# Kernel optimization log

Measured on AMD Instinct MI355X. Metric: run time of the kernel, lower is better.

The kernel has to match this reference:

```python
import jax, jax.numpy as jnp
import numpy as np
import math

B, S, D, H, F = 4, 1024, 1024, 16, 4096
NUM_BUCKETS, MAX_DISTANCE = 32, 128
LN_EPS = 1e-5


def _relative_position_bucket(relative_position, num_buckets=NUM_BUCKETS, max_distance=MAX_DISTANCE):
    # bidirectional T5 bucketing, faithful to the torch source
    n = -relative_position
    num_buckets = num_buckets // 2  # 16
    ret = (n < 0).astype(jnp.int32) * num_buckets
    n = jnp.abs(n)
    max_exact = num_buckets // 2  # 8
    is_small = n < max_exact
    val_if_large = max_exact + (
        jnp.log(jnp.maximum(n, 1).astype(jnp.float32) / max_exact)
        / math.log(max_distance / max_exact)
        * (num_buckets - max_exact)
    ).astype(jnp.int32)
    val_if_large = jnp.minimum(val_if_large, num_buckets - 1)
    return ret + jnp.where(is_small, n, val_if_large)


def layer_norm(x, g, b):
    mu = jnp.mean(x, axis=-1, keepdims=True)
    var = jnp.mean((x - mu) ** 2, axis=-1, keepdims=True)
    return g * (x - mu) / jnp.sqrt(var + LN_EPS) + b


def setup_inputs() -> dict:
    key = jax.random.key(0)
    ks = jax.random.split(key, 12)
    s = 0.02
    return {
        "in_state": jax.random.normal(ks[0], (B, S, D), jnp.float32),
        "padding_mask": jnp.ones((B, S), jnp.int32),
        "Wq": jax.random.normal(ks[1], (D, D), jnp.float32) * s,
        "bq": jnp.zeros((D,), jnp.float32),
        "Wk": jax.random.normal(ks[2], (D, D), jnp.float32) * s,
        "bk": jnp.zeros((D,), jnp.float32),
        "Wv": jax.random.normal(ks[3], (D, D), jnp.float32) * s,
        "bv": jnp.zeros((D,), jnp.float32),
        "Wo": jax.random.normal(ks[4], (D, D), jnp.float32) * s,
        "bo": jnp.zeros((D,), jnp.float32),
        "rel_bias": jax.random.normal(ks[5], (NUM_BUCKETS, H), jnp.float32) * s,
        "ln1_g": jnp.ones((D,), jnp.float32),
        "ln1_b": jnp.zeros((D,), jnp.float32),
        "W1": jax.random.normal(ks[6], (D, F), jnp.float32) * s,
        "b1": jnp.zeros((F,), jnp.float32),
        "W2": jax.random.normal(ks[7], (F, D), jnp.float32) * s,
        "b2": jnp.zeros((D,), jnp.float32),
        "ln2_g": jnp.ones((D,), jnp.float32),
        "ln2_b": jnp.zeros((D,), jnp.float32),
    }


def reference(in_state, padding_mask, Wq, bq, Wk, bk, Wv, bv, Wo, bo, rel_bias,
              ln1_g, ln1_b, W1, b1, W2, b2, ln2_g, ln2_b):
    b, s, d = in_state.shape
    dh = d // H
    q = in_state @ Wq + bq
    k = in_state @ Wk + bk
    v = in_state @ Wv + bv
    # faithful to torch's q.view(B*H, S, d_head) flat reshape (no head transpose)
    qh = q.reshape(b * H, s, dh)
    kh = k.reshape(b * H, s, dh)
    vh = v.reshape(b * H, s, dh)
    scores = jnp.einsum('bqd,bkd->bqk', qh, kh)  # no 1/sqrt(d) scaling (T5 style)
    # relative position bias: [H, S, S] tiled over batch -> block index b*H+h gets head h
    rel_pos = jnp.arange(s)[:, None] - jnp.arange(s)[None, :]
    buckets = _relative_position_bucket(rel_pos)
    bias = rel_bias[buckets].transpose(2, 0, 1)  # [H, S, S]
    bias = jnp.tile(bias, (b, 1, 1))  # [B*H, S, S]
    # padding mask: log(0/1) -> -inf/0; block b*H+h uses mask[b, value_index]
    pad = jnp.log(padding_mask.astype(jnp.float32))  # [B, S]
    pad = jnp.repeat(pad, H, axis=0)[:, None, :]  # [B*H, 1, S]
    attw = jax.nn.softmax(scores + bias + pad, axis=-1)
    att = (attw @ vh).reshape(b, s, d)
    att = att @ Wo + bo
    h = layer_norm(att + in_state, ln1_g, ln1_b)
    ff = jnp.maximum(h @ W1 + b1, 0.0) @ W2 + b2
    out = layer_norm(ff + h, ln2_g, ln2_b)
    return out
```

## Files before the change

kernel.cpp:

```cpp
#include <hip/hip_runtime.h>
#include <hip/hip_bf16.h>

typedef unsigned short u16;
typedef __attribute__((ext_vector_type(8))) short bhalf8;
typedef __attribute__((ext_vector_type(4))) float f32x4;

#define DEV __device__ __forceinline__

DEV float bf2f(u16 u) { union { unsigned int i; float f; } c; c.i = ((unsigned int)u) << 16; return c.f; }
DEV u16 f2bf(float f) {
  union { float f; unsigned int i; } c; c.f = f;
  unsigned int x = c.i;
  x += 0x7fffu + ((x >> 16) & 1u);
  return (u16)(x >> 16);
}

DEV void async16(const void* g, void* l) {
  __builtin_amdgcn_global_load_lds((__attribute__((address_space(1))) void*)g,
                                   (__attribute__((address_space(3))) void*)l, 16, 0, 0);
}

DEV void atom_pk_bf16(void* p, unsigned int v) {
  asm volatile("global_atomic_pk_add_bf16 %0, %1, off" :: "v"(p), "v"(v) : "memory");
}

struct Ptr11 { const void* p[11]; };
struct TC4 { const void* in[4]; u16* out[4]; };

__global__ void detect_kernel(const unsigned int* __restrict__ x, int* __restrict__ flag) {
  int t = threadIdx.x;
  int cnt = 0;
  for (int i = t; i < 256; i += 64) {
    unsigned int w = x[i];
    int e = (w >> 7) & 0xFF;
    if (e >= 96 && e <= 134) cnt++;
  }
#pragma unroll
  for (int o = 1; o < 64; o <<= 1) cnt += __shfl_xor(cnt, o, 64);
  if (t == 0) *flag = (cnt >= 192) ? 1 : 0;
}

DEV bhalf8 load8B(const void* base, size_t e, int isbf) {
  if (isbf) return *(const bhalf8*)((const u16*)base + e);
  const float* f = (const float*)base + e;
  float4 a = *(const float4*)f;
  float4 b = *(const float4*)(f + 4);
  bhalf8 r;
  r[0] = (short)f2bf(a.x); r[1] = (short)f2bf(a.y); r[2] = (short)f2bf(a.z); r[3] = (short)f2bf(a.w);
  r[4] = (short)f2bf(b.x); r[5] = (short)f2bf(b.y); r[6] = (short)f2bf(b.z); r[7] = (short)f2bf(b.w);
  return r;
}

__global__ __launch_bounds__(256) void convert_x(const void* __restrict__ x,
                                                 u16* __restrict__ dst,
                                                 const int* __restrict__ flag) {
  int c = blockIdx.x * 256 + threadIdx.x;
  u16* d = dst + (size_t)c * 4;
  if (*flag) {
    *(ushort4*)d = ((const ushort4*)x)[c];
  } else {
    float4 v = ((const float4*)x)[c];
    d[0] = f2bf(v.x); d[1] = f2bf(v.y); d[2] = f2bf(v.z); d[3] = f2bf(v.w);
  }
}

__global__ __launch_bounds__(256) void convert_small(Ptr11 s, float* __restrict__ dst,
                                                     const int* __restrict__ flag) {
  const int isbf = *flag;
  const int SZ[11] = {1024,1024,1024,1024,512,1024,1024,4096,1024,1024,1024};
  for (int i = threadIdx.x; i < 13824; i += 256) {
    int acc = 0, seg = -1, off = 0;
#pragma unroll
    for (int s2 = 0; s2 < 11; ++s2) {
      if (seg < 0 && i < acc + SZ[s2]) { seg = s2; off = i - acc; }
      acc += SZ[s2];
    }
    dst[i] = isbf ? bf2f(((const u16*)s.p[seg])[off]) : ((const float*)s.p[seg])[off];
  }
}

__global__ __launch_bounds__(256) void bias_init(const float* __restrict__ bias,
                                                 u16* __restrict__ out) {
  const int row = blockIdx.x, t = threadIdx.x;
  float4 bv = *(const float4*)(bias + t * 4);
  ushort4 ov; ov.x = f2bf(bv.x); ov.y = f2bf(bv.y); ov.z = f2bf(bv.z); ov.w = f2bf(bv.w);
  *(ushort4*)(out + (size_t)row * 1024 + t * 4) = ov;
}

DEV void tconv_tile(const void* in, u16* out, int R, int C, int isbf) {
  __shared__ __align__(16) u16 tile[64][72];
  const int t = threadIdx.x;
  const int c0 = blockIdx.x * 64, r0 = blockIdx.y * 64;
#pragma unroll
  for (int r = 0; r < 2; ++r) {
    int idx = r * 256 + t;
    int ri = idx >> 3, cc = (idx & 7) * 8;
    bhalf8 v = load8B(in, (size_t)(r0 + ri) * C + c0 + cc, isbf);
    *(bhalf8*)(&tile[ri][cc]) = v;
  }
  __syncthreads();
#pragma unroll
  for (int r = 0; r < 2; ++r) {
    int idx = r * 256 + t;
    int co = idx >> 3, rc = (idx & 7) * 8;
    bhalf8 v;
#pragma unroll
    for (int ii = 0; ii < 8; ++ii) v[ii] = (short)tile[rc + ii][co];
    *(bhalf8*)(out + (size_t)(c0 + co) * R + r0 + rc) = v;
  }
}

__global__ __launch_bounds__(256) void tconv_w4(TC4 p, const int* __restrict__ flag) {
  int z = blockIdx.z;
  tconv_tile(p.in[z], p.out[z], 1024, 1024, *flag);
}

__global__ __launch_bounds__(256) void tconv_generic(const void* in, u16* out, int R, int C,
                                                     const int* __restrict__ flag) {
  tconv_tile(in, out, R, C, *flag);
}

__global__ __launch_bounds__(256) void transpose_generic(const u16* in, u16* out, int R, int C) {
  __shared__ __align__(16) u16 tile[64][72];
  const int t = threadIdx.x;
  const int c0 = blockIdx.x * 64, r0 = blockIdx.y * 64;
  size_t bs = (size_t)R * C * blockIdx.z;
#pragma unroll
  for (int r = 0; r < 2; ++r) {
    int idx = r * 256 + t;
    int ri = idx >> 3, cc = (idx & 7) * 8;
    *(bhalf8*)(&tile[ri][cc]) = *(const bhalf8*)(in + bs + (size_t)(r0 + ri) * C + c0 + cc);
  }
  __syncthreads();
#pragma unroll
  for (int r = 0; r < 2; ++r) {
    int idx = r * 256 + t;
    int co = idx >> 3, rc = (idx & 7) * 8;
    bhalf8 v;
#pragma unroll
    for (int ii = 0; ii < 8; ++ii) v[ii] = (short)tile[rc + ii][co];
    *(bhalf8*)(out + bs + (size_t)(c0 + co) * R + r0 + rc) = v;
  }
}

#define MFMA_BF16(a, b, c) __builtin_amdgcn_mfma_f32_16x16x32_bf16(a, b, c, 0, 0, 0)

template<int RELU, int ATOMIC>
__global__ __launch_bounds__(512) void gemm256(
    const u16* __restrict__ A, const u16* __restrict__ BT0,
    const float* __restrict__ b0, const float* __restrict__ b1, const float* __restrict__ b2,
    u16* __restrict__ C0, int M, int N, int ldk, int kext, long sBT, long sC)
{
  __shared__ __align__(16) u16 ldsAll[65536];
  (void)M;

  const int t = threadIdx.x;
  const int wv = t >> 6, l = t & 63;
  const int wm = wv >> 2, wn = wv & 3;
  const int m0 = blockIdx.y * 256, n0 = blockIdx.x * 256;
  const int z = blockIdx.z;

  const u16* BT; const float* bias; u16* C; int koff;
  if (ATOMIC) {
    BT = BT0; bias = b0; C = C0; koff = z * kext;
  } else {
    BT = BT0 + (long)z * sBT;
    bias = (z == 0) ? b0 : (z == 1 ? b1 : b2);
    C = C0 + (long)z * sC;
    koff = 0;
  }

  const int ri = t >> 3;
  const int slc8 = (((t & 7) ^ (ri & 7)) << 3);
  const u16* agp = A + (size_t)(m0 + ri) * ldk + koff + slc8;
  const int rB = ((ri >> 5) << 6) | (ri & 31);
  const u16* bgp = BT + (size_t)(n0 + rB) * ldk + koff + slc8;

  char* lbase = (char*)ldsAll;
  char* ldst = lbase + wv * 1024;

#define STG_A(bufb, h, j, kt) async16(agp + (size_t)((j) * 128 + (h) * 64) * ldk + (size_t)(kt) * 64, \
                                      ldst + (bufb) * 32768 + (h) * 16384 + (j) * 8192)
#define STG_B(bufb, h, j, kt) async16(bgp + (size_t)((j) * 128 + (h) * 32) * ldk + (size_t)(kt) * 64, \
                                      ldst + 65536 + (bufb) * 32768 + (h) * 16384 + (j) * 8192)

  int offA[4][2], offB[2][2];
#pragma unroll
  for (int mi = 0; mi < 4; ++mi)
#pragma unroll
    for (int s = 0; s < 2; ++s)
      offA[mi][s] = wm * 8192 + (mi * 16 + (l & 15)) * 128 + ((((s << 2) + (l >> 4)) ^ (l & 7)) << 4);
#pragma unroll
  for (int nj = 0; nj < 2; ++nj)
#pragma unroll
    for (int s = 0; s < 2; ++s)
      offB[nj][s] = 65536 + wn * 4096 + (nj * 16 + (l & 15)) * 128 + ((((s << 2) + (l >> 4)) ^ (l & 7)) << 4);

  const int NT = kext >> 6;
  f32x4 acc[8][4] = {};

  STG_A(0, 0, 0, 0); STG_A(0, 0, 1, 0);
  STG_B(0, 0, 0, 0); STG_B(0, 0, 1, 0);
  STG_B(0, 1, 0, 0); STG_B(0, 1, 1, 0);
  STG_A(0, 1, 0, 0); STG_A(0, 1, 1, 0);
  if (NT > 1) {
    STG_A(1, 0, 0, 1); STG_A(1, 0, 1, 1);
    STG_B(1, 0, 0, 1); STG_B(1, 0, 1, 1);
    STG_B(1, 1, 0, 1); STG_B(1, 1, 1, 1);
    asm volatile("s_waitcnt vmcnt(6)" ::: "memory");
  } else {
    asm volatile("s_waitcnt vmcnt(0)" ::: "memory");
  }
  __builtin_amdgcn_s_barrier();

  for (int tt = 0; tt < NT; ++tt) {
    const int bf = tt & 1;
    const int bo = bf << 15;
    bhalf8 af[4][2], p0[2][2], p1[2][2];

#pragma unroll
    for (int mi = 0; mi < 4; ++mi)
#pragma unroll
      for (int s = 0; s < 2; ++s)
        af[mi][s] = *(const bhalf8*)(lbase + bo + offA[mi][s]);
#pragma unroll
    for (int nj = 0; nj < 2; ++nj)
#pragma unroll
      for (int s = 0; s < 2; ++s)
        p0[nj][s] = *(const bhalf8*)(lbase + bo + offB[nj][s]);
    if (tt + 1 < NT) { STG_A(bf ^ 1, 1, 0, tt + 1); STG_A(bf ^ 1, 1, 1, tt + 1); }
    __builtin_amdgcn_s_barrier();
    asm volatile("s_waitcnt lgkmcnt(0)" ::: "memory");
    __builtin_amdgcn_s_setprio(1);
#pragma unroll
    for (int mi = 0; mi < 4; ++mi)
#pragma unroll
      for (int nj = 0; nj < 2; ++nj) {
        acc[mi][nj] = MFMA_BF16(af[mi][0], p0[nj][0], acc[mi][nj]);
        acc[mi][nj] = MFMA_BF16(af[mi][1], p0[nj][1], acc[mi][nj]);
      }
    __builtin_amdgcn_s_setprio(0);
    __builtin_amdgcn_s_barrier();

#pragma unroll
    for (int nj = 0; nj < 2; ++nj)
#pragma unroll
      for (int s = 0; s < 2; ++s)
        p1[nj][s] = *(const bhalf8*)(lbase + bo + 16384 + offB[nj][s]);
    if (tt + 2 < NT) { STG_A(bf, 0, 0, tt + 2); STG_A(bf, 0, 1, tt + 2); }
    __builtin_amdgcn_s_barrier();
    asm volatile("s_waitcnt lgkmcnt(0)" ::: "memory");
    __builtin_amdgcn_s_setprio(1);
#pragma unroll
    for (int mi = 0; mi < 4; ++mi)
#pragma unroll
      for (int nj = 0; nj < 2; ++nj) {
        acc[mi][2 + nj] = MFMA_BF16(af[mi][0], p1[nj][0], acc[mi][2 + nj]);
        acc[mi][2 + nj] = MFMA_BF16(af[mi][1], p1[nj][1], acc[mi][2 + nj]);
      }
    __builtin_amdgcn_s_setprio(0);
    __builtin_amdgcn_s_barrier();

#pragma unroll
    for (int mi = 0; mi < 4; ++mi)
#pragma unroll
      for (int s = 0; s < 2; ++s)
        af[mi][s] = *(const bhalf8*)(lbase + bo + 16384 + offA[mi][s]);
    if (tt + 2 < NT) { STG_B(bf, 0, 0, tt + 2); STG_B(bf, 0, 1, tt + 2); }
    __builtin_amdgcn_s_barrier();
    asm volatile("s_waitcnt lgkmcnt(0)" ::: "memory");
    __builtin_amdgcn_s_setprio(1);
#pragma unroll
    for (int mi = 0; mi < 4; ++mi)
#pragma unroll
      for (int nj = 0; nj < 2; ++nj) {
        acc[4 + mi][2 + nj] = MFMA_BF16(af[mi][0], p1[nj][0], acc[4 + mi][2 + nj]);
        acc[4 + mi][2 + nj] = MFMA_BF16(af[mi][1], p1[nj][1], acc[4 + mi][2 + nj]);
      }
    __builtin_amdgcn_s_setprio(0);
    __builtin_amdgcn_s_barrier();

    if (tt + 2 < NT) { STG_B(bf, 1, 0, tt + 2); STG_B(bf, 1, 1, tt + 2); }
    __builtin_amdgcn_s_barrier();
    __builtin_amdgcn_s_setprio(1);
#pragma unroll
    for (int mi = 0; mi < 4; ++mi)
#pragma unroll
      for (int nj = 0; nj < 2; ++nj) {
        acc[4 + mi][nj] = MFMA_BF16(af[mi][0], p0[nj][0], acc[4 + mi][nj]);
        acc[4 + mi][nj] = MFMA_BF16(af[mi][1], p0[nj][1], acc[4 + mi][nj]);
      }
    __builtin_amdgcn_s_setprio(0);
    if (tt < NT - 2) {
      asm volatile("s_waitcnt vmcnt(6)" ::: "memory");
    } else if (tt == NT - 2) {
      asm volatile("s_waitcnt vmcnt(0)" ::: "memory");
    }
    __builtin_amdgcn_s_barrier();
  }
#undef STG_A
#undef STG_B

  const int lr = (l >> 4) << 2, lcc = l & 15;
  if (ATOMIC) {
#pragma unroll
    for (int nj = 0; nj < 4; ++nj) {
      int col = n0 + wn * 64 + nj * 16 + lcc;
#pragma unroll
      for (int mi = 0; mi < 8; ++mi) {
#pragma unroll
        for (int r = 0; r < 4; ++r) {
          int row = m0 + wm * 128 + mi * 16 + lr + r;
          float vo = acc[mi][nj][r];
          float vn = __shfl_xor(vo, 1, 64);
          if (!(l & 1)) {
            unsigned int pk = (unsigned int)f2bf(vo) | ((unsigned int)f2bf(vn) << 16);
            atom_pk_bf16((void*)(C + (size_t)row * N + col), pk);
          }
        }
      }
    }
  } else {
#pragma unroll
    for (int nj = 0; nj < 4; ++nj) {
      int col = n0 + wn * 64 + nj * 16 + lcc;
      float bb = bias[col];
#pragma unroll
      for (int mi = 0; mi < 8; ++mi) {
#pragma unroll
        for (int r = 0; r < 4; ++r) {
          int row = m0 + wm * 128 + mi * 16 + lr + r;
          float v = acc[mi][nj][r] + bb;
          if (RELU) v = fmaxf(v, 0.0f);
          C[(size_t)row * N + col] = f2bf(v);
        }
      }
    }
  }
}

template<int RELU>
__global__ __launch_bounds__(512) void gemm_bt(
    const u16* __restrict__ A, const u16* __restrict__ BT0,
    const float* __restrict__ b0, const float* __restrict__ b1, const float* __restrict__ b2,
    u16* __restrict__ C0, int M, int N, int K, long sBT, long sC)
{
  __shared__ __align__(16) u16 ldsA[128 * 32];
  __shared__ __align__(16) u16 ldsB[128 * 32];

  const int t = threadIdx.x;
  const int wv = t >> 6, l = t & 63;
  const int wm = wv >> 2, wn = wv & 3;
  const int m0 = blockIdx.y * 128, n0 = blockIdx.x * 128;
  const int z = blockIdx.z;

  const u16* BT = BT0 + (long)z * sBT;
  const float* bias = (z == 0) ? b0 : (z == 1 ? b1 : b2);
  u16* C = C0 + (long)z * sC;

  const int mm_s = t >> 2, kc_s = (t & 3) ^ ((t >> 4) & 3);
  const u16* agp = A + (size_t)(m0 + mm_s) * K + kc_s * 8;
  const u16* bgp = BT + (size_t)(n0 + mm_s) * K + kc_s * 8;
  char* la = (char*)ldsA + wv * 1024;
  char* lb = (char*)ldsB + wv * 1024;

  int a_off[4], b_off[2];
#pragma unroll
  for (int i = 0; i < 4; ++i) {
    int mm = wm * 64 + i * 16 + (l & 15);
    a_off[i] = (mm * 4 + ((l >> 4) ^ ((mm >> 2) & 3))) * 8;
  }
#pragma unroll
  for (int j = 0; j < 2; ++j) {
    int nn = wn * 32 + j * 16 + (l & 15);
    b_off[j] = (nn * 4 + ((l >> 4) ^ ((nn >> 2) & 3))) * 8;
  }

  f32x4 acc[4][2] = {};

  for (int kt = 0; kt < K; kt += 32) {
    __syncthreads();
    async16(agp + kt, la);
    async16(bgp + kt, lb);
    __syncthreads();

    bhalf8 af[4], bfr[2];
#pragma unroll
    for (int i = 0; i < 4; ++i) af[i] = *(const bhalf8*)(ldsA + a_off[i]);
#pragma unroll
    for (int j = 0; j < 2; ++j) bfr[j] = *(const bhalf8*)(ldsB + b_off[j]);
#pragma unroll
    for (int mi = 0; mi < 4; ++mi)
#pragma unroll
      for (int nj = 0; nj < 2; ++nj)
        acc[mi][nj] = __builtin_amdgcn_mfma_f32_16x16x32_bf16(af[mi], bfr[nj], acc[mi][nj], 0, 0, 0);
  }

  const int lr = (l >> 4) << 2, lc = l & 15;
#pragma unroll
  for (int nj = 0; nj < 2; ++nj) {
    int col = n0 + wn * 32 + nj * 16 + lc;
    float bb = bias[col];
#pragma unroll
    for (int mi = 0; mi < 4; ++mi) {
#pragma unroll
      for (int r = 0; r < 4; ++r) {
        int row = m0 + wm * 64 + mi * 16 + lr + r;
        float v = acc[mi][nj][r] + bb;
        if (RELU) v = fmaxf(v, 0.0f);
        C[(size_t)row * N + col] = f2bf(v);
      }
    }
  }
}

template<int RELU>
__global__ __launch_bounds__(256) void gemm_bn(
    const u16* __restrict__ A, const void* __restrict__ B,
    const float* __restrict__ bias, u16* __restrict__ C, int M, int N, int K,
    const int* __restrict__ flag)
{
  __shared__ __align__(16) u16 ldsA[128][40];
  __shared__ __align__(16) u16 ldsB[128][40];

  const int isbf = *flag;
  const int t = threadIdx.x;
  const int wv = t >> 6, l = t & 63;
  const int wm = wv & 1, wn = wv >> 1;
  const int m0 = blockIdx.y * 128, n0 = blockIdx.x * 128;

  const int srow = t >> 1, scol = (t & 1) * 16;
  const u16* agp = A + (size_t)(m0 + srow) * K + scol;

  const int kk = t >> 3;
  const int nn = (t & 7) * 16;

  f32x4 acc[4][4] = {};

  for (int kt = 0; kt < K; kt += 32) {
    bhalf8 a0 = *(const bhalf8*)(agp + kt);
    bhalf8 a1 = *(const bhalf8*)(agp + kt + 8);
    size_t e0 = (size_t)(kt + kk) * N + n0 + nn;
    bhalf8 b0v = load8B(B, e0, isbf);
    bhalf8 b1v = load8B(B, e0 + 8, isbf);
    __syncthreads();
    *(bhalf8*)(&ldsA[srow][scol])     = a0;
    *(bhalf8*)(&ldsA[srow][scol + 8]) = a1;
#pragma unroll
    for (int j = 0; j < 8; ++j) ldsB[nn + j][kk]     = (u16)b0v[j];
#pragma unroll
    for (int j = 0; j < 8; ++j) ldsB[nn + 8 + j][kk] = (u16)b1v[j];
    __syncthreads();

    bhalf8 af[4], bfr[4];
#pragma unroll
    for (int i = 0; i < 4; ++i)
      af[i] = *(const bhalf8*)(&ldsA[wm * 64 + i * 16 + (l & 15)][(l >> 4) * 8]);
#pragma unroll
    for (int i = 0; i < 4; ++i)
      bfr[i] = *(const bhalf8*)(&ldsB[wn * 64 + i * 16 + (l & 15)][(l >> 4) * 8]);
#pragma unroll
    for (int mi = 0; mi < 4; ++mi)
#pragma unroll
      for (int ni = 0; ni < 4; ++ni)
        acc[mi][ni] = __builtin_amdgcn_mfma_f32_16x16x32_bf16(af[mi], bfr[ni], acc[mi][ni], 0, 0, 0);
  }

  const int lr = (l >> 4) << 2, lc = l & 15;
#pragma unroll
  for (int ni = 0; ni < 4; ++ni) {
    int col = n0 + wn * 64 + ni * 16 + lc;
    float bb = bias[col];
#pragma unroll
    for (int mi = 0; mi < 4; ++mi) {
#pragma unroll
      for (int r = 0; r < 4; ++r) {
        int row = m0 + wm * 64 + mi * 16 + lr + r;
        float v = acc[mi][ni][r] + bb;
        if (RELU) v = fmaxf(v, 0.0f);
        C[(size_t)row * N + col] = f2bf(v);
      }
    }
  }
}

__global__ __launch_bounds__(256) void lut_kernel(const float* __restrict__ rbc, float* __restrict__ lut) {
  int idx = blockIdx.x * 256 + threadIdx.x;
  if (idx >= 16 * 2047) return;
  int h = idx / 2047;
  int dp = idx - h * 2047;
  int delta = dp - 1023;
  int n = -delta;
  int ret = 0;
  if (n < 0) { ret = 16; n = -n; }
  int bkt;
  if (n < 8) bkt = n;
  else {
    float v = logf((float)n * 0.125f) / logf(16.0f) * 8.0f;
    bkt = 8 + (int)v;
    if (bkt > 15) bkt = 15;
  }
  lut[idx] = (rbc[(ret + bkt) * 16 + h] - 12.0f) * 1.44269504f;
}

__global__ __launch_bounds__(256) void attn_fused(
    const u16* __restrict__ q, const u16* __restrict__ k, const u16* __restrict__ vt,
    const int* __restrict__ mask, const float* __restrict__ lut, u16* __restrict__ att)
{
  __shared__ __align__(16) u16 ldsQ[64][72];
  __shared__ __align__(16) u16 ldsK[64][72];
  __shared__ __align__(16) u16 ldsV[64][72];
  __shared__ __align__(16) u16 ldsP[4][16][72];
  __shared__ float ldsLut[2047];
  __shared__ float ldsPad[64];

  const int t = threadIdx.x;
  const int wv = t >> 6, l = t & 63;
  const int bh = blockIdx.x, qt = blockIdx.y;
  const int b = bh >> 4, h = bh & 15;
  const size_t base = (size_t)bh * 65536;
  const int q0 = qt * 64;

  for (int i = t; i < 2047; i += 256) ldsLut[i] = lut[h * 2047 + i];

  const int sr = t >> 2, sc = (t & 3) * 16;
  {
    bhalf8 q0v = *(const bhalf8*)(q + base + (size_t)(q0 + sr) * 64 + sc);
    bhalf8 q1v = *(const bhalf8*)(q + base + (size_t)(q0 + sr) * 64 + sc + 8);
    *(bhalf8*)(&ldsQ[sr][sc])     = q0v;
    *(bhalf8*)(&ldsQ[sr][sc + 8]) = q1v;
  }
  __syncthreads();

  bhalf8 qf[2];
  {
    int mm = wv * 16 + (l & 15);
#pragma unroll
    for (int s = 0; s < 2; ++s)
      qf[s] = *(const bhalf8*)(&ldsQ[mm][s * 32 + (l >> 4) * 8]);
  }

  float ls_part[4] = {0.0f, 0.0f, 0.0f, 0.0f};
  f32x4 acc_o[4] = {};

  const int* mrow = mask + b * 1024;

  for (int kt = 0; kt < 16; ++kt) {
    const int k0 = kt * 64;
    bhalf8 k0v = *(const bhalf8*)(k + base + (size_t)(k0 + sr) * 64 + sc);
    bhalf8 k1v = *(const bhalf8*)(k + base + (size_t)(k0 + sr) * 64 + sc + 8);
    bhalf8 v0v = *(const bhalf8*)(vt + base + (size_t)sr * 1024 + k0 + sc);
    bhalf8 v1v = *(const bhalf8*)(vt + base + (size_t)sr * 1024 + k0 + sc + 8);
    __syncthreads();
    *(bhalf8*)(&ldsK[sr][sc])     = k0v;
    *(bhalf8*)(&ldsK[sr][sc + 8]) = k1v;
    *(bhalf8*)(&ldsV[sr][sc])     = v0v;
    *(bhalf8*)(&ldsV[sr][sc + 8]) = v1v;
    if (t < 64) {
      int mv = mrow[k0 + t];
      ldsPad[t] = (mv > 0) ? __log2f((float)mv) : -1e30f;
    }
    __syncthreads();

    f32x4 accS[4] = {};
#pragma unroll
    for (int s = 0; s < 2; ++s) {
#pragma unroll
      for (int ni = 0; ni < 4; ++ni) {
        int nnj = ni * 16 + (l & 15);
        bhalf8 kf = *(const bhalf8*)(&ldsK[nnj][s * 32 + (l >> 4) * 8]);
        accS[ni] = __builtin_amdgcn_mfma_f32_16x16x32_bf16(qf[s], kf, accS[ni], 0, 0, 0);
      }
    }

    float padv[4];
#pragma unroll
    for (int ni = 0; ni < 4; ++ni) padv[ni] = ldsPad[ni * 16 + (l & 15)];
    const int ib = q0 + wv * 16 + ((l >> 4) << 2);
#pragma unroll
    for (int r = 0; r < 4; ++r) {
      int i_l = ((l >> 4) << 2) + r;
#pragma unroll
      for (int ni = 0; ni < 4; ++ni) {
        int j_l = ni * 16 + (l & 15);
        float s = fmaf(accS[ni][r], 1.44269504f, ldsLut[(ib + r) - (k0 + j_l) + 1023]) + padv[ni];
        float p = exp2f(s);
        ls_part[r] += p;
        ldsP[wv][i_l][j_l] = f2bf(p);
      }
    }

#pragma unroll
    for (int s = 0; s < 2; ++s) {
      int mm = l & 15;
      bhalf8 pf = *(const bhalf8*)(&ldsP[wv][mm][s * 32 + (l >> 4) * 8]);
#pragma unroll
      for (int ni = 0; ni < 4; ++ni) {
        int e = ni * 16 + (l & 15);
        bhalf8 vf = *(const bhalf8*)(&ldsV[e][s * 32 + (l >> 4) * 8]);
        acc_o[ni] = __builtin_amdgcn_mfma_f32_16x16x32_bf16(pf, vf, acc_o[ni], 0, 0, 0);
      }
    }
  }

#pragma unroll
  for (int r = 0; r < 4; ++r) {
#pragma unroll
    for (int off = 1; off < 16; off <<= 1) ls_part[r] += __shfl_xor(ls_part[r], off, 64);
    ls_part[r] = 1.0f / ls_part[r];
  }

#pragma unroll
  for (int ni = 0; ni < 4; ++ni) {
#pragma unroll
    for (int r = 0; r < 4; ++r) {
      int i = q0 + wv * 16 + ((l >> 4) << 2) + r;
      int e = ni * 16 + (l & 15);
      att[base + (size_t)i * 64 + e] = f2bf(acc_o[ni][r] * ls_part[r]);
    }
  }
}

template<int LAST>
__global__ __launch_bounds__(256) void ln_kernel(
    const u16* __restrict__ x, const u16* __restrict__ res,
    const float* __restrict__ g, const float* __restrict__ b,
    void* __restrict__ out, const int* __restrict__ flag)
{
  const int row = blockIdx.x, t = threadIdx.x;
  const size_t off = (size_t)row * 1024 + t * 4;
  ushort4 xv = *(const ushort4*)(x + off);
  ushort4 rv = *(const ushort4*)(res + off);
  float v0 = bf2f(xv.x) + bf2f(rv.x);
  float v1 = bf2f(xv.y) + bf2f(rv.y);
  float v2 = bf2f(xv.z) + bf2f(rv.z);
  float v3 = bf2f(xv.w) + bf2f(rv.w);
  float s = v0 + v1 + v2 + v3;
  float sq = v0 * v0 + v1 * v1 + v2 * v2 + v3 * v3;
#pragma unroll
  for (int o = 1; o < 64; o <<= 1) { s += __shfl_xor(s, o, 64); sq += __shfl_xor(sq, o, 64); }
  __shared__ float red[8];
  const int wv = t >> 6, l = t & 63;
  if (l == 0) { red[wv] = s; red[4 + wv] = sq; }
  __syncthreads();
  s = red[0] + red[1] + red[2] + red[3];
  sq = red[4] + red[5] + red[6] + red[7];
  float mu = s * 0.0009765625f;
  float var = sq * 0.0009765625f - mu * mu;
  float rstd = rsqrtf(var + 1e-5f);
  float4 gv = *(const float4*)(g + t * 4);
  float4 bv = *(const float4*)(b + t * 4);
  float o0 = gv.x * (v0 - mu) * rstd + bv.x;
  float o1 = gv.y * (v1 - mu) * rstd + bv.y;
  float o2 = gv.z * (v2 - mu) * rstd + bv.z;
  float o3 = gv.w * (v3 - mu) * rstd + bv.w;
  if (!LAST) {
    ushort4 ov; ov.x = f2bf(o0); ov.y = f2bf(o1); ov.z = f2bf(o2); ov.w = f2bf(o3);
    *(ushort4*)((u16*)out + off) = ov;
  } else {
    if (*flag) {
      ushort4 ov; ov.x = f2bf(o0); ov.y = f2bf(o1); ov.z = f2bf(o2); ov.w = f2bf(o3);
      *(ushort4*)((u16*)out + off) = ov;
    } else {
      float4 ov; ov.x = o0; ov.y = o1; ov.z = o2; ov.w = o3;
      *(float4*)((float*)out + off) = ov;
    }
  }
}

extern "C" void kernel_launch(void* const* d_in, const int* in_sizes, int n_in,
                              void* d_out, int out_size, void* d_ws, size_t ws_size,
                              hipStream_t stream) {
  const void* x  = d_in[0];
  const int* mask = (const int*)d_in[1];
  const void* Wq = d_in[2];  const void* bq = d_in[3];
  const void* Wk = d_in[4];  const void* bk = d_in[5];
  const void* Wv = d_in[6];  const void* bv = d_in[7];
  const void* Wo = d_in[8];  const void* bo = d_in[9];
  const void* rb = d_in[10];
  const void* g1 = d_in[11]; const void* be1 = d_in[12];
  const void* W1 = d_in[13]; const void* b1 = d_in[14];
  const void* W2 = d_in[15]; const void* b2 = d_in[16];
  const void* g2 = d_in[17]; const void* be2 = d_in[18];

  char* ws = (char*)d_ws;
  const size_t MB = 1024 * 1024;
  const bool FAST = (ws_size >= 57 * MB);

  const size_t TAIL = FAST ? 56 * MB : 48 * MB;
  float* smalls = (float*)(ws + TAIL);
  float* lut    = (float*)(ws + TAIL + 56 * 1024);
  int*   flag   = (int*)(ws + TAIL + 192 * 1024);

  float* bqc  = smalls + 0;
  float* bkc  = smalls + 1024;
  float* bvc  = smalls + 2048;
  float* boc  = smalls + 3072;
  float* rbc  = smalls + 4096;
  float* g1c  = smalls + 4608;
  float* be1c = smalls + 5632;
  float* b1c  = smalls + 6656;
  float* b2c  = smalls + 10752;
  float* g2c  = smalls + 11776;
  float* be2c = smalls + 12800;

  detect_kernel<<<1, 64, 0, stream>>>((const unsigned int*)x, flag);
  Ptr11 sml;
  sml.p[0] = bq; sml.p[1] = bk; sml.p[2] = bv; sml.p[3] = bo; sml.p[4] = rb;
  sml.p[5] = g1; sml.p[6] = be1; sml.p[7] = b1; sml.p[8] = b2; sml.p[9] = g2; sml.p[10] = be2;
  convert_small<<<1, 256, 0, stream>>>(sml, smalls, flag);
  lut_kernel<<<dim3(128), 256, 0, stream>>>(rbc, lut);

  if (FAST) {
    u16* xc   = (u16*)(ws + 0 * MB);
    u16* WqT  = (u16*)(ws + 8 * MB);
    u16* WkT  = WqT + 1048576;
    u16* WvT  = WqT + 2 * 1048576;
    u16* WoT  = WqT + 3 * 1048576;
    u16* qb   = (u16*)(ws + 16 * MB);
    u16* kb   = (u16*)(ws + 24 * MB);
    u16* vb   = (u16*)(ws + 32 * MB);
    u16* vtb  = (u16*)(ws + 40 * MB);
    u16* attb = (u16*)(ws + 32 * MB);
    u16* xo   = (u16*)(ws + 16 * MB);
    u16* hb   = (u16*)(ws + 48 * MB);
    u16* W1T  = (u16*)(ws + 8 * MB);
    u16* W2T  = (u16*)(ws + 0 * MB);
    u16* ff1  = (u16*)(ws + 16 * MB);
    u16* ff2o = (u16*)(ws + 8 * MB);

    convert_x<<<4096, 256, 0, stream>>>(x, xc, flag);
    TC4 tw; tw.in[0] = Wq; tw.in[1] = Wk; tw.in[2] = Wv; tw.in[3] = Wo;
    tw.out[0] = WqT; tw.out[1] = WkT; tw.out[2] = WvT; tw.out[3] = WoT;
    tconv_w4<<<dim3(16, 16, 4), 256, 0, stream>>>(tw, flag);

    gemm_bt<0><<<dim3(8, 32, 3), 512, 0, stream>>>(xc, WqT, bqc, bkc, bvc, qb,
                                                   4096, 1024, 1024, 1048576L, 4194304L);
    transpose_generic<<<dim3(1, 16, 64), 256, 0, stream>>>(vb, vtb, 1024, 64);
    attn_fused<<<dim3(64, 16), 256, 0, stream>>>(qb, kb, vtb, mask, lut, attb);
    gemm_bt<0><<<dim3(8, 32, 1), 512, 0, stream>>>(attb, WoT, boc, boc, boc, xo,
                                                   4096, 1024, 1024, 0L, 0L);
    tconv_generic<<<dim3(64, 16), 256, 0, stream>>>(W1, W1T, 1024, 4096, flag);
    ln_kernel<0><<<dim3(4096), 256, 0, stream>>>(xo, xc, g1c, be1c, hb, flag);
    tconv_generic<<<dim3(16, 64), 256, 0, stream>>>(W2, W2T, 4096, 1024, flag);
    gemm256<1, 0><<<dim3(16, 16, 1), 512, 0, stream>>>(hb, W1T, b1c, b1c, b1c, ff1,
                                                       4096, 4096, 1024, 1024, 0L, 0L);
    bias_init<<<dim3(4096), 256, 0, stream>>>(b2c, ff2o);
    gemm256<0, 1><<<dim3(4, 16, 4), 512, 0, stream>>>(ff1, W2T, b2c, b2c, b2c, ff2o,
                                                      4096, 1024, 4096, 1024, 0L, 0L);
    ln_kernel<1><<<dim3(4096), 256, 0, stream>>>(ff2o, hb, g2c, be2c, d_out, flag);
  } else {
    u16* xc   = (u16*)(ws + 0 * MB);
    u16* WqT  = (u16*)(ws + 8 * MB);
    u16* WkT  = WqT + 1048576;
    u16* WvT  = WqT + 2 * 1048576;
    u16* WoT  = WqT + 3 * 1048576;
    u16* qb   = (u16*)(ws + 16 * MB);
    u16* kb   = (u16*)(ws + 24 * MB);
    u16* vb   = (u16*)(ws + 32 * MB);
    u16* vtb  = (u16*)(ws + 40 * MB);
    u16* attb = (u16*)(ws + 32 * MB);
    u16* xo   = (u16*)(ws + 16 * MB);
    u16* hb   = (u16*)(ws + 40 * MB);
    u16* ff1  = (u16*)(ws + 0 * MB);
    u16* ff2o = (u16*)(ws + 32 * MB);

    convert_x<<<4096, 256, 0, stream>>>(x, xc, flag);
    TC4 tw; tw.in[0] = Wq; tw.in[1] = Wk; tw.in[2] = Wv; tw.in[3] = Wo;
    tw.out[0] = WqT; tw.out[1] = WkT; tw.out[2] = WvT; tw.out[3] = WoT;
    tconv_w4<<<dim3(16, 16, 4), 256, 0, stream>>>(tw, flag);

    gemm_bt<0><<<dim3(8, 32, 3), 512, 0, stream>>>(xc, WqT, bqc, bkc, bvc, qb,
                                                   4096, 1024, 1024, 1048576L, 4194304L);
    transpose_generic<<<dim3(1, 16, 64), 256, 0, stream>>>(vb, vtb, 1024, 64);
    attn_fused<<<dim3(64, 16), 256, 0, stream>>>(qb, kb, vtb, mask, lut, attb);
    gemm_bt<0><<<dim3(8, 32, 1), 512, 0, stream>>>(attb, WoT, boc, boc, boc, xo,
                                                   4096, 1024, 1024, 0L, 0L);
    ln_kernel<0><<<dim3(4096), 256, 0, stream>>>(xo, xc, g1c, be1c, hb, flag);
    gemm_bn<1><<<dim3(32, 32), 256, 0, stream>>>(hb, W1, b1c, ff1, 4096, 4096, 1024, flag);
    gemm_bn<0><<<dim3(8, 32), 256, 0, stream>>>(ff1, W2, b2c, ff2o, 4096, 1024, 4096, flag);
    ln_kernel<1><<<dim3(4096), 256, 0, stream>>>(ff2o, hb, g2c, be2c, d_out, flag);
  }
}
```

Baseline: 445.1 us.

## Use separate LDS arrays in gemm256 and route QKV/out-proj GEMMs through it

```diff
diff --git a/kernel.cpp b/kernel.cpp
--- a/kernel.cpp
+++ b/kernel.cpp
@@ -151,7 +151,8 @@
     const float* __restrict__ b0, const float* __restrict__ b1, const float* __restrict__ b2,
     u16* __restrict__ C0, int M, int N, int ldk, int kext, long sBT, long sC)
 {
-  __shared__ __align__(16) u16 ldsAll[65536];
+  __shared__ __align__(16) u16 A0h0[8192], A0h1[8192], A1h0[8192], A1h1[8192];
+  __shared__ __align__(16) u16 B0h0[8192], B0h1[8192], B1h0[8192], B1h1[8192];
   (void)M;
 
   const int t = threadIdx.x;
@@ -176,13 +177,10 @@
   const int rB = ((ri >> 5) << 6) | (ri & 31);
   const u16* bgp = BT + (size_t)(n0 + rB) * ldk + koff + slc8;
 
-  char* lbase = (char*)ldsAll;
-  char* ldst = lbase + wv * 1024;
-
-#define STG_A(bufb, h, j, kt) async16(agp + (size_t)((j) * 128 + (h) * 64) * ldk + (size_t)(kt) * 64, \
-                                      ldst + (bufb) * 32768 + (h) * 16384 + (j) * 8192)
-#define STG_B(bufb, h, j, kt) async16(bgp + (size_t)((j) * 128 + (h) * 32) * ldk + (size_t)(kt) * 64, \
-                                      ldst + 65536 + (bufb) * 32768 + (h) * 16384 + (j) * 8192)
+#define STGA(ARR, h, j, kt) async16(agp + (size_t)((j) * 128 + (h) * 64) * ldk + (size_t)(kt) * 64, \
+                                    (char*)(ARR) + (j) * 8192 + wv * 1024)
+#define STGB(ARR, h, j, kt) async16(bgp + (size_t)((j) * 128 + (h) * 32) * ldk + (size_t)(kt) * 64, \
+                                    (char*)(ARR) + (j) * 8192 + wv * 1024)
 
   int offA[4][2], offB[2][2];
 #pragma unroll
@@ -194,112 +192,98 @@
   for (int nj = 0; nj < 2; ++nj)
 #pragma unroll
     for (int s = 0; s < 2; ++s)
-      offB[nj][s] = 65536 + wn * 4096 + (nj * 16 + (l & 15)) * 128 + ((((s << 2) + (l >> 4)) ^ (l & 7)) << 4);
+      offB[nj][s] = wn * 4096 + (nj * 16 + (l & 15)) * 128 + ((((s << 2) + (l >> 4)) ^ (l & 7)) << 4);
 
   const int NT = kext >> 6;
   f32x4 acc[8][4] = {};
 
-  STG_A(0, 0, 0, 0); STG_A(0, 0, 1, 0);
-  STG_B(0, 0, 0, 0); STG_B(0, 0, 1, 0);
-  STG_B(0, 1, 0, 0); STG_B(0, 1, 1, 0);
-  STG_A(0, 1, 0, 0); STG_A(0, 1, 1, 0);
+  STGA(A0h0, 0, 0, 0); STGA(A0h0, 0, 1, 0);
+  STGB(B0h0, 0, 0, 0); STGB(B0h0, 0, 1, 0);
+  STGB(B0h1, 1, 0, 0); STGB(B0h1, 1, 1, 0);
+  STGA(A0h1, 1, 0, 0); STGA(A0h1, 1, 1, 0);
   if (NT > 1) {
-    STG_A(1, 0, 0, 1); STG_A(1, 0, 1, 1);
-    STG_B(1, 0, 0, 1); STG_B(1, 0, 1, 1);
-    STG_B(1, 1, 0, 1); STG_B(1, 1, 1, 1);
+    STGA(A1h0, 0, 0, 1); STGA(A1h0, 0, 1, 1);
+    STGB(B1h0, 0, 0, 1); STGB(B1h0, 0, 1, 1);
+    STGB(B1h1, 1, 0, 1); STGB(B1h1, 1, 1, 1);
     asm volatile("s_waitcnt vmcnt(6)" ::: "memory");
   } else {
     asm volatile("s_waitcnt vmcnt(0)" ::: "memory");
   }
   __builtin_amdgcn_s_barrier();
 
-  for (int tt = 0; tt < NT; ++tt) {
-    const int bf = tt & 1;
-    const int bo = bf << 15;
-    bhalf8 af[4][2], p0[2][2], p1[2][2];
-
-#pragma unroll
-    for (int mi = 0; mi < 4; ++mi)
-#pragma unroll
-      for (int s = 0; s < 2; ++s)
-        af[mi][s] = *(const bhalf8*)(lbase + bo + offA[mi][s]);
-#pragma unroll
-    for (int nj = 0; nj < 2; ++nj)
-#pragma unroll
-      for (int s = 0; s < 2; ++s)
-        p0[nj][s] = *(const bhalf8*)(lbase + bo + offB[nj][s]);
-    if (tt + 1 < NT) { STG_A(bf ^ 1, 1, 0, tt + 1); STG_A(bf ^ 1, 1, 1, tt + 1); }
-    __builtin_amdgcn_s_barrier();
-    asm volatile("s_waitcnt lgkmcnt(0)" ::: "memory");
-    __builtin_amdgcn_s_setprio(1);
-#pragma unroll
-    for (int mi = 0; mi < 4; ++mi)
-#pragma unroll
-      for (int nj = 0; nj < 2; ++nj) {
-        acc[mi][nj] = MFMA_BF16(af[mi][0], p0[nj][0], acc[mi][nj]);
-        acc[mi][nj] = MFMA_BF16(af[mi][1], p0[nj][1], acc[mi][nj]);
-      }
-    __builtin_amdgcn_s_setprio(0);
-    __builtin_amdgcn_s_barrier();
-
-#pragma unroll
-    for (int nj = 0; nj < 2; ++nj)
-#pragma unroll
-      for (int s = 0; s < 2; ++s)
-        p1[nj][s] = *(const bhalf8*)(lbase + bo + 16384 + offB[nj][s]);
-    if (tt + 2 < NT) { STG_A(bf, 0, 0, tt + 2); STG_A(bf, 0, 1, tt + 2); }
-    __builtin_amdgcn_s_barrier();
-    asm volatile("s_waitcnt lgkmcnt(0)" ::: "memory");
-    __builtin_amdgcn_s_setprio(1);
-#pragma unroll
-    for (int mi = 0; mi < 4; ++mi)
-#pragma unroll
-      for (int nj = 0; nj < 2; ++nj) {
-        acc[mi][2 + nj] = MFMA_BF16(af[mi][0], p1[nj][0], acc[mi][2 + nj]);
-        acc[mi][2 + nj] = MFMA_BF16(af[mi][1], p1[nj][1], acc[mi][2 + nj]);
-      }
-    __builtin_amdgcn_s_setprio(0);
-    __builtin_amdgcn_s_barrier();
-
-#pragma unroll
-    for (int mi = 0; mi < 4; ++mi)
-#pragma unroll
-      for (int s = 0; s < 2; ++s)
-        af[mi][s] = *(const bhalf8*)(lbase + bo + 16384 + offA[mi][s]);
-    if (tt + 2 < NT) { STG_B(bf, 0, 0, tt + 2); STG_B(bf, 0, 1, tt + 2); }
-    __builtin_amdgcn_s_barrier();
-    asm volatile("s_waitcnt lgkmcnt(0)" ::: "memory");
-    __builtin_amdgcn_s_setprio(1);
-#pragma unroll
-    for (int mi = 0; mi < 4; ++mi)
-#pragma unroll
-      for (int nj = 0; nj < 2; ++nj) {
-        acc[4 + mi][2 + nj] = MFMA_BF16(af[mi][0], p1[nj][0], acc[4 + mi][2 + nj]);
-        acc[4 + mi][2 + nj] = MFMA_BF16(af[mi][1], p1[nj][1], acc[4 + mi][2 + nj]);
-      }
-    __builtin_amdgcn_s_setprio(0);
-    __builtin_amdgcn_s_barrier();
-
-    if (tt + 2 < NT) { STG_B(bf, 1, 0, tt + 2); STG_B(bf, 1, 1, tt + 2); }
-    __builtin_amdgcn_s_barrier();
-    __builtin_amdgcn_s_setprio(1);
-#pragma unroll
-    for (int mi = 0; mi < 4; ++mi)
-#pragma unroll
-      for (int nj = 0; nj < 2; ++nj) {
-        acc[4 + mi][nj] = MFMA_BF16(af[mi][0], p0[nj][0], acc[4 + mi][nj]);
-        acc[4 + mi][nj] = MFMA_BF16(af[mi][1], p0[nj][1], acc[4 + mi][nj]);
-      }
-    __builtin_amdgcn_s_setprio(0);
-    if (tt < NT - 2) {
-      asm volatile("s_waitcnt vmcnt(6)" ::: "memory");
-    } else if (tt == NT - 2) {
-      asm volatile("s_waitcnt vmcnt(0)" ::: "memory");
-    }
-    __builtin_amdgcn_s_barrier();
-  }
-#undef STG_A
-#undef STG_B
+#define ITER(TT, CA0, CA1, CB0, CB1, NA1)                                        \
+  {                                                                              \
+    bhalf8 af[4][2], p0[2][2], p1[2][2];                                         \
+                      \
+    _Pragma("unroll") for (int mi = 0; mi < 4; ++mi)                             \
+      _Pragma("unroll") for (int s = 0; s < 2; ++s)                              \
+        af[mi][s] = *(const bhalf8*)((const char*)(CA0) + offA[mi][s]);          \
+    _Pragma("unroll") for (int nj = 0; nj < 2; ++nj)                             \
+      _Pragma("unroll") for (int s = 0; s < 2; ++s)                              \
+        p0[nj][s] = *(const bhalf8*)((const char*)(CB0) + offB[nj][s]);          \
+    if ((TT) + 1 < NT) { STGA(NA1, 1, 0, (TT) + 1); STGA(NA1, 1, 1, (TT) + 1); } \
+    __builtin_amdgcn_s_barrier();                                                \
+    asm volatile("s_waitcnt lgkmcnt(0)" ::: "memory");                           \
+    __builtin_amdgcn_s_setprio(1);                                               \
+    _Pragma("unroll") for (int mi = 0; mi < 4; ++mi)                             \
+      _Pragma("unroll") for (int nj = 0; nj < 2; ++nj) {                         \
+        acc[mi][nj] = MFMA_BF16(af[mi][0], p0[nj][0], acc[mi][nj]);              \
+        acc[mi][nj] = MFMA_BF16(af[mi][1], p0[nj][1], acc[mi][nj]);              \
+      }                                                                          \
+    __builtin_amdgcn_s_setprio(0);                                               \
+    __builtin_amdgcn_s_barrier();                                                \
+                           \
+    _Pragma("unroll") for (int nj = 0; nj < 2; ++nj)                             \
+      _Pragma("unroll") for (int s = 0; s < 2; ++s)                              \
+        p1[nj][s] = *(const bhalf8*)((const char*)(CB1) + offB[nj][s]);          \
+    if ((TT) + 2 < NT) { STGA(CA0, 0, 0, (TT) + 2); STGA(CA0, 0, 1, (TT) + 2); } \
+    __builtin_amdgcn_s_barrier();                                                \
+    asm volatile("s_waitcnt lgkmcnt(0)" ::: "memory");                           \
+    __builtin_amdgcn_s_setprio(1);                                               \
+    _Pragma("unroll") for (int mi = 0; mi < 4; ++mi)                             \
+      _Pragma("unroll") for (int nj = 0; nj < 2; ++nj) {                         \
+        acc[mi][2 + nj] = MFMA_BF16(af[mi][0], p1[nj][0], acc[mi][2 + nj]);      \
+        acc[mi][2 + nj] = MFMA_BF16(af[mi][1], p1[nj][1], acc[mi][2 + nj]);      \
+      }                                                                          \
+    __builtin_amdgcn_s_setprio(0);                                               \
+    __builtin_amdgcn_s_barrier();                                                \
+                           \
+    _Pragma("unroll") for (int mi = 0; mi < 4; ++mi)                             \
+      _Pragma("unroll") for (int s = 0; s < 2; ++s)                              \
+        af[mi][s] = *(const bhalf8*)((const char*)(CA1) + offA[mi][s]);          \
+    if ((TT) + 2 < NT) { STGB(CB0, 0, 0, (TT) + 2); STGB(CB0, 0, 1, (TT) + 2); } \
+    __builtin_amdgcn_s_barrier();                                                \
+    asm volatile("s_waitcnt lgkmcnt(0)" ::: "memory");                           \
+    __builtin_amdgcn_s_setprio(1);                                               \
+    _Pragma("unroll") for (int mi = 0; mi < 4; ++mi)                             \
+      _Pragma("unroll") for (int nj = 0; nj < 2; ++nj) {                         \
+        acc[4 + mi][2 + nj] = MFMA_BF16(af[mi][0], p1[nj][0], acc[4 + mi][2 + nj]); \
+        acc[4 + mi][2 + nj] = MFMA_BF16(af[mi][1], p1[nj][1], acc[4 + mi][2 + nj]); \
+      }                                                                          \
+    __builtin_amdgcn_s_setprio(0);                                               \
+    __builtin_amdgcn_s_barrier();                                                \
+                             \
+    if ((TT) + 2 < NT) { STGB(CB1, 1, 0, (TT) + 2); STGB(CB1, 1, 1, (TT) + 2); } \
+    __builtin_amdgcn_s_barrier();                                                \
+    __builtin_amdgcn_s_setprio(1);                                               \
+    _Pragma("unroll") for (int mi = 0; mi < 4; ++mi)                             \
+      _Pragma("unroll") for (int nj = 0; nj < 2; ++nj) {                         \
+        acc[4 + mi][nj] = MFMA_BF16(af[mi][0], p0[nj][0], acc[4 + mi][nj]);      \
+        acc[4 + mi][nj] = MFMA_BF16(af[mi][1], p0[nj][1], acc[4 + mi][nj]);      \
+      }                                                                          \
+    __builtin_amdgcn_s_setprio(0);                                               \
+    if ((TT) < NT - 2)       asm volatile("s_waitcnt vmcnt(6)" ::: "memory");    \
+    else if ((TT) == NT - 2) asm volatile("s_waitcnt vmcnt(0)" ::: "memory");    \
+    __builtin_amdgcn_s_barrier();                                                \
+  }
+
+  for (int tt = 0; tt < NT; tt += 2) {
+    ITER(tt,     A0h0, A0h1, B0h0, B0h1, A1h1);
+    ITER(tt + 1, A1h0, A1h1, B1h0, B1h1, A0h1);
+  }
+#undef ITER
+#undef STGA
+#undef STGB
 
   const int lr = (l >> 4) << 2, lcc = l & 15;
   if (ATOMIC) {
@@ -734,12 +718,12 @@
     tw.out[0] = WqT; tw.out[1] = WkT; tw.out[2] = WvT; tw.out[3] = WoT;
     tconv_w4<<<dim3(16, 16, 4), 256, 0, stream>>>(tw, flag);
 
-    gemm_bt<0><<<dim3(8, 32, 3), 512, 0, stream>>>(xc, WqT, bqc, bkc, bvc, qb,
-                                                   4096, 1024, 1024, 1048576L, 4194304L);
+    gemm256<0, 0><<<dim3(4, 16, 3), 512, 0, stream>>>(xc, WqT, bqc, bkc, bvc, qb,
+                                                      4096, 1024, 1024, 1024, 1048576L, 4194304L);
     transpose_generic<<<dim3(1, 16, 64), 256, 0, stream>>>(vb, vtb, 1024, 64);
     attn_fused<<<dim3(64, 16), 256, 0, stream>>>(qb, kb, vtb, mask, lut, attb);
-    gemm_bt<0><<<dim3(8, 32, 1), 512, 0, stream>>>(attb, WoT, boc, boc, boc, xo,
-                                                   4096, 1024, 1024, 0L, 0L);
+    gemm256<0, 0><<<dim3(4, 16, 1), 512, 0, stream>>>(attb, WoT, boc, boc, boc, xo,
+                                                      4096, 1024, 1024, 1024, 0L, 0L);
     tconv_generic<<<dim3(64, 16), 256, 0, stream>>>(W1, W1T, 1024, 4096, flag);
     ln_kernel<0><<<dim3(4096), 256, 0, stream>>>(xo, xc, g1c, be1c, hb, flag);
     tconv_generic<<<dim3(16, 64), 256, 0, stream>>>(W2, W2T, 4096, 1024, flag);
```

New measurement: 446.8 us. Within noise of the previous version (+0.4%).
